# Kernel optimization log

Measured on AMD Instinct MI355X. Metric: run time of the kernel, lower is better.

Reference implementation:

```python
import jax, jax.numpy as jnp
import numpy as np

FP16_MIN = -65504.0
FP16_MAX = 65504.0

B, S, D, H = 2, 2048, 1024, 16
HD = D // H


def setup_inputs() -> dict:
    key = jax.random.key(0)
    ks = jax.random.split(key, 12)
    s = 0.02
    inp = {
        "x_q": jax.random.normal(ks[0], (B, S, D), jnp.float32),
        "x_k": jax.random.normal(ks[1], (B, S, D), jnp.float32),
        "x_v": jax.random.normal(ks[2], (B, S, D), jnp.float32),
        # causal mask [B, 1, S, S]; 0 entries are masked out
        "mask": jnp.broadcast_to(jnp.tril(jnp.ones((S, S), jnp.int32)), (B, 1, S, S)),
        "Wq": jax.random.normal(ks[3], (D, D), jnp.float32) * s,
        "bq": jnp.zeros((D,), jnp.float32),
        "Wk": jax.random.normal(ks[4], (D, D), jnp.float32) * s,
        "bk": jnp.zeros((D,), jnp.float32),
        "Wv": jax.random.normal(ks[5], (D, D), jnp.float32) * s,
        "bv": jnp.zeros((D,), jnp.float32),
        "Wo": jax.random.normal(ks[6], (D, D), jnp.float32) * s,
        "bo": jnp.zeros((D,), jnp.float32),
    }
    return inp


def _split_heads(x):
    # [B, S, D] -> [B, H, S, HD]
    b, s, _ = x.shape
    return x.reshape(b, s, H, HD).transpose(0, 2, 1, 3)


def reference(x_q, x_k, x_v, mask, Wq, bq, Wk, bk, Wv, bv, Wo, bo):
    scale = jnp.sqrt(jnp.float32(HD))
    q = _split_heads(x_q @ Wq + bq)  # [B,H,S,HD]
    k = _split_heads(x_k @ Wk + bk)
    v = _split_heads(x_v @ Wv + bv)

    scores = jnp.einsum("bhqd,bhkd->bhqk", q, k) / scale  # [B,H,S,S]
    scores = jnp.where(mask == 0, FP16_MIN, scores)
    scores = jnp.where(jnp.isneginf(scores), FP16_MIN, scores)
    scores = jnp.where(jnp.isposinf(scores), FP16_MAX, scores)

    probs = jax.nn.softmax(scores, axis=-1)  # dropout p=0.0 -> identity
    ctx = jnp.einsum("bhqk,bhkd->bhqd", probs, v)  # [B,H,S,HD]
    ctx = ctx.transpose(0, 2, 1, 3).reshape(x_q.shape[0], x_q.shape[1], D)
    out = ctx @ Wo + bo
    return out, probs
```

## Files before the change

### kernel.cpp

```cpp
#include <hip/hip_runtime.h>


typedef __bf16 bf16x8 __attribute__((ext_vector_type(8)));
typedef __bf16 bf16x2 __attribute__((ext_vector_type(2)));
typedef float f32x4 __attribute__((ext_vector_type(4)));

__device__ __forceinline__ unsigned short f2bf_hw(float f) {
  return __builtin_bit_cast(unsigned short, (__bf16)f);
}
__device__ __forceinline__ unsigned int pk2bf(float a, float b) {
  bf16x2 t = {(__bf16)a, (__bf16)b};
  return __builtin_bit_cast(unsigned int, t);
}
__device__ __forceinline__ float bf2f_lo(unsigned int u) {
  return __builtin_bit_cast(float, u << 16);
}
__device__ __forceinline__ float bf2f_hi(unsigned int u) {
  return __builtin_bit_cast(float, u & 0xffff0000u);
}

__global__ void transpose_w(const float* __restrict__ W0, const float* __restrict__ W1,
                            const float* __restrict__ W2, const float* __restrict__ W3,
                            unsigned short* __restrict__ Wt) {
  __shared__ float t[32][33];
  const int z = blockIdx.z;
  const float* W = (z == 0) ? W0 : (z == 1) ? W1 : (z == 2) ? W2 : W3;
  unsigned short* o = Wt + (size_t)z * 1048576u;
  const int n0 = blockIdx.x * 32, k0 = blockIdx.y * 32;
  const int tx = threadIdx.x, ty = threadIdx.y;
#pragma unroll
  for (int i = 0; i < 4; i++)
    t[ty + 8 * i][tx] = W[(size_t)(k0 + ty + 8 * i) * 1024 + n0 + tx];
  __syncthreads();
#pragma unroll
  for (int i = 0; i < 4; i++)
    o[(size_t)(n0 + ty + 8 * i) * 1024 + k0 + tx] = f2bf_hw(t[tx][ty + 8 * i]);
}

__global__ __launch_bounds__(256) void gemm_kernel(
    const void* __restrict__ A0, const void* __restrict__ A1, const void* __restrict__ A2,
    const unsigned short* __restrict__ Wtb,
    const float* __restrict__ b0, const float* __restrict__ b1, const float* __restrict__ b2,
    void* __restrict__ O0, void* __restrict__ O1, void* __restrict__ O2,
    const int mode0) {
  __shared__ unsigned short Alds[64 * 72];
  const int z = blockIdx.z;
  const int mode = mode0 + z;
  const void* Av = (z == 0) ? A0 : (z == 1) ? A1 : A2;
  const float* bias = (z == 0) ? b0 : (z == 1) ? b1 : b2;
  void* outv = (z == 0) ? O0 : (z == 1) ? O1 : O2;
  const unsigned short* Wt = Wtb + (size_t)z * 1048576u;

  const int tid = threadIdx.x;
  const int lane = tid & 63;
  const int wave = tid >> 6;
  const int wm = wave >> 1, wn = wave & 1;
  const int m0 = blockIdx.y * 64, n0 = blockIdx.x * 128;
  const int g = lane >> 4, c = lane & 15;

  f32x4 acc[2][4];
#pragma unroll
  for (int i = 0; i < 2; i++)
#pragma unroll
    for (int j = 0; j < 4; j++) acc[i][j] = (f32x4){0.f, 0.f, 0.f, 0.f};

  const int srow = tid >> 2;
  const int sch = (tid & 3) * 16;

  uint4 pk0, pk1;
#define LOAD_PACK(KB)                                                             \
  if (mode < 3) {                                                                 \
    const float* A = (const float*)Av;                                            \
    const float4* src = (const float4*)(A + (size_t)(m0 + srow) * 1024 + (KB) + sch); \
    const float4 v0 = src[0], v1 = src[1], v2 = src[2], v3 = src[3];              \
    pk0.x = pk2bf(v0.x, v0.y);                                                    \
    pk0.y = pk2bf(v0.z, v0.w);                                                    \
    pk0.z = pk2bf(v1.x, v1.y);                                                    \
    pk0.w = pk2bf(v1.z, v1.w);                                                    \
    pk1.x = pk2bf(v2.x, v2.y);                                                    \
    pk1.y = pk2bf(v2.z, v2.w);                                                    \
    pk1.z = pk2bf(v3.x, v3.y);                                                    \
    pk1.w = pk2bf(v3.z, v3.w);                                                    \
  } else {                                                                        \
    const unsigned short* A = (const unsigned short*)Av;                          \
    const uint4* src = (const uint4*)(A + (size_t)(m0 + srow) * 1024 + (KB) + sch); \
    pk0 = src[0];                                                                 \
    pk1 = src[1];                                                                 \
  }

  LOAD_PACK(0);
  for (int kb = 0; kb < 1024; kb += 64) {
    *(uint4*)&Alds[srow * 72 + sch] = pk0;
    *(uint4*)&Alds[srow * 72 + sch + 8] = pk1;
    if (kb + 64 < 1024) { LOAD_PACK(kb + 64); }
    __syncthreads();

    bf16x8 af[2][2], bfr[4][2];
#pragma unroll
    for (int mi = 0; mi < 2; mi++)
#pragma unroll
      for (int kk = 0; kk < 2; kk++)
        af[mi][kk] = *(const bf16x8*)&Alds[(wm * 32 + mi * 16 + c) * 72 + kk * 32 + g * 8];
#pragma unroll
    for (int nf = 0; nf < 4; nf++)
#pragma unroll
      for (int kk = 0; kk < 2; kk++)
        bfr[nf][kk] = *(const bf16x8*)(Wt + (size_t)(n0 + wn * 64 + nf * 16 + c) * 1024 + kb + kk * 32 + g * 8);
#pragma unroll
    for (int kk = 0; kk < 2; kk++)
#pragma unroll
      for (int mi = 0; mi < 2; mi++)
#pragma unroll
        for (int nf = 0; nf < 4; nf++)
          acc[mi][nf] = __builtin_amdgcn_mfma_f32_16x16x32_bf16(af[mi][kk], bfr[nf][kk], acc[mi][nf], 0, 0, 0);
    __syncthreads();
  }
#undef LOAD_PACK

#pragma unroll
  for (int nf = 0; nf < 4; nf++) {
    const int col = n0 + wn * 64 + nf * 16 + c;
    const float bc = bias[col];
#pragma unroll
    for (int mi = 0; mi < 2; mi++) {
#pragma unroll
      for (int r = 0; r < 4; r++) {
        const int row = m0 + wm * 32 + mi * 16 + g * 4 + r;
        const float v = acc[mi][nf][r] + bc;
        if (mode == 0) {
          ((unsigned short*)outv)[(size_t)row * 1024 + col] = f2bf_hw(v * 0.1803368801111244f);
        } else if (mode == 1) {
          ((unsigned short*)outv)[(size_t)row * 1024 + col] = f2bf_hw(v);
        } else if (mode == 2) {
          const int bb = row >> 11, s = row & 2047;
          ((unsigned short*)outv)[((size_t)(bb * 1024 + col)) * 2048 + s] = f2bf_hw(v);
        } else {
          ((float*)outv)[(size_t)row * 1024 + col] = v;
        }
      }
    }
  }
}

__global__ __launch_bounds__(512, 4) void attn_kernel(
    const unsigned short* __restrict__ Q, const unsigned short* __restrict__ K,
    const unsigned short* __restrict__ Vt, float* __restrict__ probs,
    unsigned short* __restrict__ ctx) {
  __shared__ unsigned short Klds[2][64 * 72];
  __shared__ unsigned short Vlds[2][64 * 72];
  __shared__ unsigned short Plds[128 * 72];

  const int tid = threadIdx.x;
  const int lane = tid & 63, wave = tid >> 6;
  const int g = lane >> 4, c = lane & 15;
  const int bh = blockIdx.x;
  const int b = bh >> 4, h = bh & 15;
  const int by = blockIdx.y;
  const int qt = (by < 8) ? (15 - by) : (by - 8);
  const int q0 = qt * 128;
  const int qrow0 = q0 + wave * 16;
  const int wave_kend = qrow0 + 16;

  const unsigned short* Qh = Q + ((size_t)(b * 2048 + qrow0)) * 1024 + h * 64;
  const unsigned short* Kh = K + ((size_t)b * 2048) * 1024 + h * 64;
  const unsigned short* Vh = Vt + ((size_t)bh) * 64 * 2048;
  float* Ph = probs + ((size_t)(bh * 2048 + q0)) * 2048;

  const bf16x8 qa0 = *(const bf16x8*)&Qh[(size_t)c * 1024 + g * 8];
  const bf16x8 qa1 = *(const bf16x8*)&Qh[(size_t)c * 1024 + 32 + g * 8];

  const int srow = tid >> 3;
  const int scol = (tid & 7) * 8;
  const int kb_end = q0 + 128;

  float lp[4] = {0.f, 0.f, 0.f, 0.f};
  f32x4 cacc[4];
#pragma unroll
  for (int nf = 0; nf < 4; nf++) cacc[nf] = (f32x4){0.f, 0.f, 0.f, 0.f};

  const int prow = lane >> 2;
  const int pcb = (lane & 3) * 16;
  unsigned short* PwOut = (unsigned short*)Ph + (size_t)(wave * 16 + prow) * 4096 + pcb;
  const unsigned short* PwLds = &Plds[(wave * 16 + prow) * 72 + pcb];

  {
    *(uint4*)&Klds[0][srow * 72 + scol] = *(const uint4*)(Kh + (size_t)srow * 1024 + scol);
    *(uint4*)&Vlds[0][srow * 72 + scol] = *(const uint4*)(Vh + (size_t)srow * 2048 + scol);
  }

  int cur = 0;
  for (int kb = 0; kb < kb_end; kb += 64, cur ^= 1) {
    uint4 kn, vn;
    const bool more = (kb + 64) < kb_end;
    if (more) {
      kn = *(const uint4*)(Kh + (size_t)(kb + 64 + srow) * 1024 + scol);
      vn = *(const uint4*)(Vh + (size_t)srow * 2048 + kb + 64 + scol);
    }
    __syncthreads();
    if (more) {
      *(uint4*)&Klds[cur ^ 1][srow * 72 + scol] = kn;
      *(uint4*)&Vlds[cur ^ 1][srow * 72 + scol] = vn;
    }

    if (kb < wave_kend) {
      f32x4 sv[4];
#pragma unroll
      for (int sub = 0; sub < 4; sub++) {
        sv[sub] = (f32x4){0.f, 0.f, 0.f, 0.f};
        const unsigned short* Kr = &Klds[cur][(sub * 16 + c) * 72];
        sv[sub] = __builtin_amdgcn_mfma_f32_16x16x32_bf16(qa0, *(const bf16x8*)&Kr[g * 8], sv[sub], 0, 0, 0);
        sv[sub] = __builtin_amdgcn_mfma_f32_16x16x32_bf16(qa1, *(const bf16x8*)&Kr[32 + g * 8], sv[sub], 0, 0, 0);
      }
      if (kb + 63 > qrow0) {
#pragma unroll
        for (int sub = 0; sub < 4; sub++)
#pragma unroll
          for (int r = 0; r < 4; r++)
            if (kb + sub * 16 + c > qrow0 + g * 4 + r) sv[sub][r] = -1e30f;
      }
#pragma unroll
      for (int sub = 0; sub < 4; sub++)
#pragma unroll
        for (int r = 0; r < 4; r++) {
          const float pu = __builtin_amdgcn_exp2f(sv[sub][r]);
          lp[r] += pu;
          Plds[(wave * 16 + g * 4 + r) * 72 + sub * 16 + c] = f2bf_hw(pu);
        }
      const bf16x8 pa0 = *(const bf16x8*)&Plds[(wave * 16 + c) * 72 + g * 8];
      const bf16x8 pa1 = *(const bf16x8*)&Plds[(wave * 16 + c) * 72 + 32 + g * 8];
#pragma unroll
      for (int nf = 0; nf < 4; nf++) {
        const bf16x8 vf0 = *(const bf16x8*)&Vlds[cur][(nf * 16 + c) * 72 + g * 8];
        const bf16x8 vf1 = *(const bf16x8*)&Vlds[cur][(nf * 16 + c) * 72 + 32 + g * 8];
        cacc[nf] = __builtin_amdgcn_mfma_f32_16x16x32_bf16(pa0, vf0, cacc[nf], 0, 0, 0);
        cacc[nf] = __builtin_amdgcn_mfma_f32_16x16x32_bf16(pa1, vf1, cacc[nf], 0, 0, 0);
      }
      unsigned short* dst = PwOut + kb;
      *(uint4*)dst = *(const uint4*)PwLds;
      *(uint4*)(dst + 8) = *(const uint4*)(PwLds + 8);
    } else {
      unsigned short* dst = PwOut + kb;
      *(uint4*)dst = make_uint4(0u, 0u, 0u, 0u);
      *(uint4*)(dst + 8) = make_uint4(0u, 0u, 0u, 0u);
    }
  }

#pragma unroll
  for (int off = 1; off < 16; off <<= 1)
#pragma unroll
    for (int r = 0; r < 4; r++) lp[r] += __shfl_xor(lp[r], off);
  float invl[4];
#pragma unroll
  for (int r = 0; r < 4; r++) invl[r] = 1.0f / lp[r];

#pragma unroll
  for (int nf = 0; nf < 4; nf++)
#pragma unroll
    for (int r = 0; r < 4; r++)
      ctx[((size_t)(b * 2048 + qrow0 + g * 4 + r)) * 1024 + h * 64 + nf * 16 + c] =
          f2bf_hw(cacc[nf][r] * invl[r]);
}

__global__ __launch_bounds__(256) void norm_probs(float* __restrict__ probs) {
  __shared__ float wsum[4];
  const int rowIdx = blockIdx.x;
  const int q = rowIdx & 2047;
  const int kbe = ((q >> 7) + 1) << 7;
  float* base = probs + (size_t)rowIdx * 2048;
  const int t = threadIdx.x;
  const int c0 = t * 8;

  uint4 raw = make_uint4(0u, 0u, 0u, 0u);
  if (c0 < kbe) raw = *(const uint4*)((const unsigned short*)base + c0);
  float f0 = bf2f_lo(raw.x), f1 = bf2f_hi(raw.x), f2 = bf2f_lo(raw.y), f3 = bf2f_hi(raw.y);
  float f4 = bf2f_lo(raw.z), f5 = bf2f_hi(raw.z), f6 = bf2f_lo(raw.w), f7 = bf2f_hi(raw.w);

  float s = ((f0 + f1) + (f2 + f3)) + ((f4 + f5) + (f6 + f7));
#pragma unroll
  for (int off = 1; off < 64; off <<= 1) s += __shfl_xor(s, off);
  if ((t & 63) == 0) wsum[t >> 6] = s;
  __syncthreads();
  const float il = 1.0f / (wsum[0] + wsum[1] + wsum[2] + wsum[3]);

  float4* dst = (float4*)(base + c0);
  dst[0] = make_float4(f0 * il, f1 * il, f2 * il, f3 * il);
  dst[1] = make_float4(f4 * il, f5 * il, f6 * il, f7 * il);
}

extern "C" void kernel_launch(void* const* d_in, const int* in_sizes, int n_in,
                              void* d_out, int out_size, void* d_ws, size_t ws_size,
                              hipStream_t stream) {
  if (ws_size < (size_t)40 * 1024 * 1024) return;

  const float* xq = (const float*)d_in[0];
  const float* xk = (const float*)d_in[1];
  const float* xv = (const float*)d_in[2];
  const float* Wq = (const float*)d_in[4];
  const float* bq = (const float*)d_in[5];
  const float* Wk = (const float*)d_in[6];
  const float* bk = (const float*)d_in[7];
  const float* Wv = (const float*)d_in[8];
  const float* bv = (const float*)d_in[9];
  const float* Wo = (const float*)d_in[10];
  const float* bo = (const float*)d_in[11];

  unsigned short* ws = (unsigned short*)d_ws;
  unsigned short* Wt = ws;
  unsigned short* Qw = ws + (size_t)4 * 1048576u;
  unsigned short* Kw = Qw + 4194304u;
  unsigned short* Vtw = Kw + 4194304u;
  unsigned short* Cw = Vtw + 4194304u;

  float* out = (float*)d_out;
  float* probs = out + 4194304u;

  transpose_w<<<dim3(32, 32, 4), dim3(32, 8), 0, stream>>>(Wq, Wk, Wv, Wo, Wt);
  gemm_kernel<<<dim3(8, 64, 3), 256, 0, stream>>>(xq, xk, xv, Wt, bq, bk, bv,
                                                  Qw, Kw, Vtw, 0);
  attn_kernel<<<dim3(32, 16, 1), 512, 0, stream>>>(Qw, Kw, Vtw, probs, Cw);
  norm_probs<<<dim3(65536), 256, 0, stream>>>(probs);
  gemm_kernel<<<dim3(8, 64, 1), 256, 0, stream>>>(Cw, Cw, Cw, Wt + 3u * 1048576u,
                                                  bo, bo, bo, out, out, out, 3);
}
```

Before: 347.8 us.

## Fuse probability normalization into attention kernel epilogue

Removes the separate norm_probs launch and instead normalizes each wave's probability rows at the end of the attention kernel, reading back the unnormalized bf16 values it wrote and rewriting them as scaled fp32. Row sums come from the in-register accumulators, broadcast by shuffles, so the second pass over probs needs no block reduction. The zero-fill of fully masked key blocks is dropped because the epilogue writes zeros beyond the causal end. This saves a kernel launch and a global reduction pass, but the epilogue loop is serial per row and relies on in-place reuse of the output buffer within the same wave.

```diff
diff --git a/kernel.cpp b/kernel.cpp
--- a/kernel.cpp
+++ b/kernel.cpp
@@ -238,10 +238,6 @@
       unsigned short* dst = PwOut + kb;
       *(uint4*)dst = *(const uint4*)PwLds;
       *(uint4*)(dst + 8) = *(const uint4*)(PwLds + 8);
-    } else {
-      unsigned short* dst = PwOut + kb;
-      *(uint4*)dst = make_uint4(0u, 0u, 0u, 0u);
-      *(uint4*)(dst + 8) = make_uint4(0u, 0u, 0u, 0u);
     }
   }
 
@@ -259,32 +255,32 @@
     for (int r = 0; r < 4; r++)
       ctx[((size_t)(b * 2048 + qrow0 + g * 4 + r)) * 1024 + h * 64 + nf * 16 + c] =
           f2bf_hw(cacc[nf][r] * invl[r]);
-}
-
-__global__ __launch_bounds__(256) void norm_probs(float* __restrict__ probs) {
-  __shared__ float wsum[4];
-  const int rowIdx = blockIdx.x;
-  const int q = rowIdx & 2047;
-  const int kbe = ((q >> 7) + 1) << 7;
-  float* base = probs + (size_t)rowIdx * 2048;
-  const int t = threadIdx.x;
-  const int c0 = t * 8;
-
-  uint4 raw = make_uint4(0u, 0u, 0u, 0u);
-  if (c0 < kbe) raw = *(const uint4*)((const unsigned short*)base + c0);
-  float f0 = bf2f_lo(raw.x), f1 = bf2f_hi(raw.x), f2 = bf2f_lo(raw.y), f3 = bf2f_hi(raw.y);
-  float f4 = bf2f_lo(raw.z), f5 = bf2f_hi(raw.z), f6 = bf2f_lo(raw.w), f7 = bf2f_hi(raw.w);
-
-  float s = ((f0 + f1) + (f2 + f3)) + ((f4 + f5) + (f6 + f7));
-#pragma unroll
-  for (int off = 1; off < 64; off <<= 1) s += __shfl_xor(s, off);
-  if ((t & 63) == 0) wsum[t >> 6] = s;
-  __syncthreads();
-  const float il = 1.0f / (wsum[0] + wsum[1] + wsum[2] + wsum[3]);
-
-  float4* dst = (float4*)(base + c0);
-  dst[0] = make_float4(f0 * il, f1 * il, f2 * il, f3 * il);
-  dst[1] = make_float4(f4 * il, f5 * il, f6 * il, f7 * il);
+
+  float rs[16];
+#pragma unroll
+  for (int rr = 0; rr < 16; rr++)
+    rs[rr] = __shfl(lp[rr & 3], (rr >> 2) << 4);
+  asm volatile("s_waitcnt vmcnt(0)" ::: "memory");
+
+  const int ve = wave_kend;
+#pragma unroll 1
+  for (int rr = 0; rr < 16; rr++) {
+    const float il = 1.0f / rs[rr];
+    const unsigned short* srcb = (const unsigned short*)Ph + (size_t)(wave * 16 + rr) * 4096;
+    float* dstr = Ph + (size_t)(wave * 16 + rr) * 2048;
+    uint2 rw[8];
+#pragma unroll
+    for (int i = 0; i < 8; i++) {
+      const int col = i * 256 + lane * 4;
+      rw[i] = (col < ve) ? *(const uint2*)(srcb + col) : make_uint2(0u, 0u);
+    }
+#pragma unroll
+    for (int i = 0; i < 8; i++) {
+      const int col = i * 256 + lane * 4;
+      *(float4*)(dstr + col) = make_float4(bf2f_lo(rw[i].x) * il, bf2f_hi(rw[i].x) * il,
+                                           bf2f_lo(rw[i].y) * il, bf2f_hi(rw[i].y) * il);
+    }
+  }
 }
 
 extern "C" void kernel_launch(void* const* d_in, const int* in_sizes, int n_in,
@@ -318,7 +314,6 @@
   gemm_kernel<<<dim3(8, 64, 3), 256, 0, stream>>>(xq, xk, xv, Wt, bq, bk, bv,
                                                   Qw, Kw, Vtw, 0);
   attn_kernel<<<dim3(32, 16, 1), 512, 0, stream>>>(Qw, Kw, Vtw, probs, Cw);
-  norm_probs<<<dim3(65536), 256, 0, stream>>>(probs);
   gemm_kernel<<<dim3(8, 64, 1), 256, 0, stream>>>(Cw, Cw, Cw, Wt + 3u * 1048576u,
                                                   bo, bo, bo, out, out, out, 3);
 }
```

Measured after the change: 373.3 us. 7.3% more time.
